# Optimization experiments

Measured on AMD Instinct MI355X. Metric: run time of the kernel, lower is better.

The kernel has to match this reference:

```python
import jax, jax.numpy as jnp
import numpy as np

N_NODES = 100000
N_EDGES = 3200000
D_IN = 128
D_HID = 128
N_CLASSES = 40


def setup_inputs() -> dict:
    key = jax.random.key(0)
    ks = jax.random.split(key, 8)
    x = jax.random.normal(ks[0], (N_NODES, D_IN), dtype=jnp.float32)
    edge_index = jax.random.randint(ks[1], (2, N_EDGES), 0, N_NODES, dtype=jnp.int64)
    s1 = 1.0 / np.sqrt(D_IN)
    s2 = 1.0 / np.sqrt(D_HID)
    W1 = jax.random.normal(ks[2], (D_IN, D_HID), dtype=jnp.float32) * s1
    b1 = jnp.zeros((D_HID,), dtype=jnp.float32)
    W2 = jax.random.normal(ks[3], (D_HID, D_HID), dtype=jnp.float32) * s2
    b2 = jnp.zeros((D_HID,), dtype=jnp.float32)
    Wl = jax.random.normal(ks[4], (D_HID, N_CLASSES), dtype=jnp.float32) * s2
    bl = jnp.zeros((N_CLASSES,), dtype=jnp.float32)
    return {"x": x, "edge_index": edge_index, "W1": W1, "b1": b1,
            "W2": W2, "b2": b2, "Wl": Wl, "bl": bl}


def _gcn_conv(x, W, b, src, dst, inv_sqrt_deg, n_nodes):
    # h = X @ W  (linear transform first: cheaper when out_dim <= in_dim)
    h = x @ W  # [N, d_out]
    # symmetric normalization: norm_e = deg(src)^-1/2 * deg(dst)^-1/2
    norm = inv_sqrt_deg[src] * inv_sqrt_deg[dst]  # [E]
    msg = h[src] * norm[:, None]                  # gather + scale  [E, d_out]
    out = jax.ops.segment_sum(msg, dst, num_segments=n_nodes)  # scatter-add
    return out + b


def reference(x, edge_index, W1, b1, W2, b2, Wl, bl):
    n = x.shape[0]
    # GCNConv adds self-loops before normalization (PyG default)
    loops = jnp.arange(n, dtype=edge_index.dtype)
    src = jnp.concatenate([edge_index[0], loops])
    dst = jnp.concatenate([edge_index[1], loops])
    deg = jax.ops.segment_sum(jnp.ones_like(dst, dtype=x.dtype), dst, num_segments=n)
    inv_sqrt_deg = jnp.where(deg > 0, jax.lax.rsqrt(deg), 0.0)

    h = _gcn_conv(x, W1, b1, src, dst, inv_sqrt_deg, n)
    h = jax.nn.relu(h)
    h = _gcn_conv(h, W2, b2, src, dst, inv_sqrt_deg, n)
    h = jax.nn.relu(h)
    return h @ Wl + bl
```

## Files before the change

### kernel.cpp

```cpp
#include <hip/hip_runtime.h>
#include <hip/hip_bf16.h>

typedef _Float16 f16;
typedef _Float16 f16x8 __attribute__((ext_vector_type(8)));

#define D 128
#define N_CLS 40
#define BN 128
#define NBMAX 1024

__global__ __launch_bounds__(256) void k_hist(const int* __restrict__ dst,
                                              int* __restrict__ bcnt, int e) {
  __shared__ int lh[NBMAX];
  for (int j = threadIdx.x; j < NBMAX; j += 256) lh[j] = 0;
  __syncthreads();
  int stride = gridDim.x * blockDim.x;
  for (int q = blockIdx.x * blockDim.x + threadIdx.x; q < e; q += stride)
    atomicAdd(&lh[dst[q] >> 7], 1);
  __syncthreads();
  for (int j = threadIdx.x; j < NBMAX; j += 256)
    if (lh[j]) atomicAdd(&bcnt[j], lh[j]);
}

__global__ __launch_bounds__(1024) void k_bscan(const int* __restrict__ bcnt,
                                                int* __restrict__ bbase,
                                                int* __restrict__ bcur) {
  __shared__ int sums[NBMAX];
  int t = threadIdx.x;
  int c = bcnt[t];
  sums[t] = c;
  __syncthreads();
  for (int off = 1; off < NBMAX; off <<= 1) {
    int a = (t >= off) ? sums[t - off] : 0;
    __syncthreads();
    sums[t] += a;
    __syncthreads();
  }
  bbase[t] = sums[t] - c;
  bcur[t] = sums[t] - c;
}

__global__ __launch_bounds__(256) void k_place(const int* __restrict__ src,
                                               const int* __restrict__ dst,
                                               int* __restrict__ bcur,
                                               unsigned int* __restrict__ binned,
                                               int e, int nwg) {
  __shared__ int lh[NBMAX];
  __shared__ int lofs[NBMAX];
  __shared__ int lcur[NBMAX];
  int chunk = (e + nwg - 1) / nwg;
  int lo = blockIdx.x * chunk;
  int hi = min(e, lo + chunk);
  int t = threadIdx.x;
  for (int j = t; j < NBMAX; j += 256) { lh[j] = 0; lcur[j] = 0; }
  __syncthreads();
  for (int q = lo + t; q < hi; q += 256) atomicAdd(&lh[dst[q] >> 7], 1);
  __syncthreads();
  for (int j = t; j < NBMAX; j += 256) {
    int c = lh[j];
    lofs[j] = c ? atomicAdd(&bcur[j], c) : 0;
  }
  __syncthreads();
  for (int q = lo + t; q < hi; q += 256) {
    int d = dst[q];
    int b = d >> 7;
    int r = atomicAdd(&lcur[b], 1);
    binned[lofs[b] + r] = ((unsigned int)(d & 127) << 17) | (unsigned int)src[q];
  }
}

__global__ __launch_bounds__(256) void k_csr(const unsigned int* __restrict__ binned,
                                             const int* __restrict__ bbase,
                                             int* __restrict__ csr,
                                             int* __restrict__ deg,
                                             float* __restrict__ isd,
                                             int* __restrict__ row_start, int n) {
  int b = blockIdx.x;
  int lo = bbase[b], hi = bbase[b + 1];
  __shared__ int h[BN];
  __shared__ int sc[BN];
  __shared__ int cur[BN];
  int t = threadIdx.x;
  if (t < BN) h[t] = 0;
  __syncthreads();
  for (int q = lo + t; q < hi; q += 256) atomicAdd(&h[binned[q] >> 17], 1);
  __syncthreads();
  if (t < BN) sc[t] = h[t];
  __syncthreads();
  for (int off = 1; off < BN; off <<= 1) {
    int a = 0;
    if (t < BN && t >= off) a = sc[t - off];
    __syncthreads();
    if (t < BN) sc[t] += a;
    __syncthreads();
  }
  if (t < BN) {
    int excl = sc[t] - h[t];
    cur[t] = lo + excl;
    int i = b * BN + t;
    if (i < n) {
      deg[i] = h[t];
      isd[i] = rsqrtf((float)(h[t] + 1));
      row_start[i] = lo + excl;
    }
  }
  __syncthreads();
  for (int q = lo + t; q < hi; q += 256) {
    unsigned int u = binned[q];
    int p = atomicAdd(&cur[u >> 17], 1);
    csr[p] = (int)(u & 0x1FFFF);
  }
}

template <bool HALF_IN>
__global__ __launch_bounds__(256) void k_gemm_t(const void* __restrict__ Xv,
                                                const float* __restrict__ W,
                                                const float* __restrict__ isd,
                                                f16* __restrict__ HS, int n) {
  __shared__ float Xt[64][D + 4];
  __shared__ float Wb[32][D + 4];
  int t = threadIdx.x;
  int r0 = blockIdx.x * 64;
  if (!HALF_IN) {
    const float* X = (const float*)Xv;
    for (int q = t; q < 64 * 32; q += 256) {
      int row = q >> 5, cb = (q & 31) << 2;
      float4 v = {0.f, 0.f, 0.f, 0.f};
      if (r0 + row < n) v = *(const float4*)(X + (size_t)(r0 + row) * D + cb);
      *(float4*)&Xt[row][cb] = v;
    }
  } else {
    const f16* X = (const f16*)Xv;
    for (int q = t; q < 64 * 16; q += 256) {
      int row = q >> 4, cb = (q & 15) << 3;
      f16x8 v = 0;
      if (r0 + row < n) v = *(const f16x8*)(X + (size_t)(r0 + row) * D + cb);
      float* xp = &Xt[row][cb];
#pragma unroll
      for (int j = 0; j < 8; ++j) xp[j] = (float)v[j];
    }
  }
  int tr = ((t >> 4) & 15) << 2;
  int tc = (t & 15) << 3;
  float acc[4][8];
#pragma unroll
  for (int i = 0; i < 4; ++i)
#pragma unroll
    for (int j = 0; j < 8; ++j) acc[i][j] = 0.f;

  for (int hh = 0; hh < 4; ++hh) {
    __syncthreads();
    for (int q = t; q < 32 * 32; q += 256) {
      int row = q >> 5, cb = (q & 31) << 2;
      *(float4*)&Wb[row][cb] = *(const float4*)(W + (size_t)(hh * 32 + row) * D + cb);
    }
    __syncthreads();
#pragma unroll 4
    for (int k = 0; k < 32; ++k) {
      float4 u0 = *(const float4*)&Wb[k][tc];
      float4 u1 = *(const float4*)&Wb[k][tc + 4];
      float bv[8] = {u0.x, u0.y, u0.z, u0.w, u1.x, u1.y, u1.z, u1.w};
      int kk = hh * 32 + k;
#pragma unroll
      for (int i = 0; i < 4; ++i) {
        float a = Xt[tr + i][kk];
#pragma unroll
        for (int j = 0; j < 8; ++j) acc[i][j] += a * bv[j];
      }
    }
  }
#pragma unroll
  for (int i = 0; i < 4; ++i) {
    int row = r0 + tr + i;
    if (row < n) {
      float s = isd[row];
      f16x8 ov;
#pragma unroll
      for (int j = 0; j < 8; ++j) ov[j] = (f16)(s * acc[i][j]);
      *(f16x8*)(HS + (size_t)row * D + tc) = ov;
    }
  }
}

__device__ inline void gather8(const f16* __restrict__ HS,
                               const int* __restrict__ csr,
                               int start, int c, int lane, float acc[8]) {
  int g = lane >> 4;
  int l = lane & 15;
  const char* base = (const char*)HS;
  size_t lofs = (size_t)(l << 4);
#pragma unroll
  for (int j = 0; j < 8; ++j) acc[j] = 0.f;

  for (int e0 = 0; e0 < c; e0 += 64) {
    int nb = min(64, c - e0);
    int idx = (lane < nb) ? csr[start + e0 + lane] : 0;
    int kb = 0;
    for (; kb + 16 <= nb; kb += 16) {
      f16x8 a16 = 0;
#pragma unroll
      for (int k = 0; k < 16; k += 4) {
        int s = __shfl(idx, kb + k + g);
        a16 += *(const f16x8*)(base + (((size_t)s) << 8) + lofs);
      }
#pragma unroll
      for (int j = 0; j < 8; ++j) acc[j] += (float)a16[j];
    }
    if (kb < nb) {
      f16x8 a16 = 0;
      for (int k = kb; k < nb; k += 4) {
        int kk = k + g;
        int s = __shfl(idx, kk);
        f16x8 u = *(const f16x8*)(base + (((size_t)s) << 8) + lofs);
        if (kk < nb) a16 += u;
      }
#pragma unroll
      for (int j = 0; j < 8; ++j) acc[j] += (float)a16[j];
    }
  }
#pragma unroll
  for (int j = 0; j < 8; ++j) {
    float v = acc[j];
    v += __shfl_xor(v, 16);
    v += __shfl_xor(v, 32);
    acc[j] = v;
  }
}

__global__ __launch_bounds__(64) void k_agg1(const f16* __restrict__ HS,
                                             const int* __restrict__ csr,
                                             const int* __restrict__ row_start,
                                             const int* __restrict__ deg,
                                             const float* __restrict__ isd,
                                             const float* __restrict__ bias,
                                             f16* __restrict__ G) {
  int i = blockIdx.x;
  int lane = threadIdx.x;
  int l = lane & 15;
  float acc[8];
  gather8(HS, csr, row_start[i], deg[i], lane, acc);
  f16x8 sv = *(const f16x8*)(HS + (size_t)i * D + l * 8);
  float di = isd[i];
  float4 bb0 = *(const float4*)(bias + l * 8);
  float4 bb1 = *(const float4*)(bias + l * 8 + 4);
  float bv[8] = {bb0.x, bb0.y, bb0.z, bb0.w, bb1.x, bb1.y, bb1.z, bb1.w};
  f16x8 ov;
#pragma unroll
  for (int j = 0; j < 8; ++j) {
    float v = di * (acc[j] + (float)sv[j]) + bv[j];
    v = v > 0.f ? v : 0.f;
    ov[j] = (f16)v;
  }
  if ((lane >> 4) == 0) *(f16x8*)(G + (size_t)i * D + l * 8) = ov;
}

__global__ __launch_bounds__(64) void k_agg_cls(const f16* __restrict__ HS,
                                                const int* __restrict__ csr,
                                                const int* __restrict__ row_start,
                                                const int* __restrict__ deg,
                                                const float* __restrict__ isd,
                                                const float* __restrict__ b2,
                                                const float* __restrict__ Wl,
                                                const float* __restrict__ bl,
                                                float* __restrict__ out) {
  int i = blockIdx.x;
  int lane = threadIdx.x;
  int l = lane & 15;
  float acc[8];
  gather8(HS, csr, row_start[i], deg[i], lane, acc);
  f16x8 sv = *(const f16x8*)(HS + (size_t)i * D + l * 8);
  float di = isd[i];
  float4 bb0 = *(const float4*)(b2 + l * 8);
  float4 bb1 = *(const float4*)(b2 + l * 8 + 4);
  float bv[8] = {bb0.x, bb0.y, bb0.z, bb0.w, bb1.x, bb1.y, bb1.z, bb1.w};
  __shared__ float tt[D];
#pragma unroll
  for (int j = 0; j < 8; ++j) {
    float v = di * (acc[j] + (float)sv[j]) + bv[j];
    bv[j] = v > 0.f ? v : 0.f;
  }
  if ((lane >> 4) == 0) {
    *(float4*)&tt[l * 8] = make_float4(bv[0], bv[1], bv[2], bv[3]);
    *(float4*)&tt[l * 8 + 4] = make_float4(bv[4], bv[5], bv[6], bv[7]);
  }
  __syncthreads();
  if (lane < N_CLS) {
    float o = bl[lane];
#pragma unroll 8
    for (int k = 0; k < D; ++k) o += tt[k] * Wl[k * N_CLS + lane];
    out[(size_t)i * N_CLS + lane] = o;
  }
}

extern "C" void kernel_launch(void* const* d_in, const int* in_sizes, int n_in,
                              void* d_out, int out_size, void* d_ws, size_t ws_size,
                              hipStream_t stream) {
  const float* x  = (const float*)d_in[0];
  const int*   ei = (const int*)d_in[1];
  const float* W1 = (const float*)d_in[2];
  const float* b1 = (const float*)d_in[3];
  const float* W2 = (const float*)d_in[4];
  const float* b2 = (const float*)d_in[5];
  const float* Wl = (const float*)d_in[6];
  const float* bl = (const float*)d_in[7];
  float* out = (float*)d_out;

  const int n = in_sizes[0] / D;
  const int e = in_sizes[1] / 2;
  const int* src = ei;
  const int* dst = ei + e;
  const int nb = (n + BN - 1) / BN;

  char* ws = (char*)d_ws;
  size_t off = 0;
  auto alloc = [&](size_t bytes) -> void* {
    void* p = ws + off;
    off += (bytes + 255) & ~(size_t)255;
    return p;
  };
  int*   bcnt      = (int*)alloc(NBMAX * 4);
  int*   bbase     = (int*)alloc(NBMAX * 4);
  int*   bcur      = (int*)alloc(NBMAX * 4);
  int*   deg       = (int*)alloc((size_t)n * 4);
  int*   row_start = (int*)alloc((size_t)n * 4);
  float* isd       = (float*)alloc((size_t)n * 4);
  int*   csr       = (int*)alloc((size_t)e * 4);
  f16*   hA        = (f16*)alloc((size_t)n * D * 2);
  f16*   hB        = (f16*)alloc((size_t)n * D * 2);
  unsigned int* binned = (unsigned int*)hA;

  hipMemsetAsync(bcnt, 0, NBMAX * 4, stream);

  const int nwg_place = 512;
  k_hist<<<1024, 256, 0, stream>>>(dst, bcnt, e);
  k_bscan<<<1, 1024, 0, stream>>>(bcnt, bbase, bcur);
  k_place<<<nwg_place, 256, 0, stream>>>(src, dst, bcur, binned, e, nwg_place);
  k_csr<<<nb, 256, 0, stream>>>(binned, bbase, csr, deg, isd, row_start, n);

  int gblocks = (n + 63) / 64;
  k_gemm_t<false><<<gblocks, 256, 0, stream>>>(x, W1, isd, hA, n);
  k_agg1<<<n, 64, 0, stream>>>(hA, csr, row_start, deg, isd, b1, hB);
  k_gemm_t<true><<<gblocks, 256, 0, stream>>>(hB, W2, isd, hA, n);
  k_agg_cls<<<n, 64, 0, stream>>>(hA, csr, row_start, deg, isd, b2, Wl, bl, out);
}
```

Measured before the change: 570.3 us.

## Rework gather to issue 8 independent row loads per lane, pack 4 nodes per block

The neighbor gather no longer loads 64 indices cooperatively and broadcasts them by shuffle. Each lane now reads its own 8 CSR indices directly, using clamped addresses, then issues 8 independent 16-byte row loads before summing in fp16 pairs. This raises memory-level parallelism per wave for average degree about 33. Both aggregation kernels now pack 4 nodes (one per wave) into 256-thread blocks, and the classifier loop reads the shared hidden vector as float4. The trade-offs are more redundant index loads, loads wasted on partial tails, and fp16 partial sums of 4 values before conversion to fp32.

```diff
diff --git a/kernel.cpp b/kernel.cpp
--- a/kernel.cpp
+++ b/kernel.cpp
@@ -185,64 +185,59 @@
 __device__ inline void gather8(const f16* __restrict__ HS,
                                const int* __restrict__ csr,
                                int start, int c, int lane, float acc[8]) {
-  int g = lane >> 4;
+  const int g = lane >> 4;
+  const char* base = (const char*)HS + ((lane & 15) << 4);
+  const int* __restrict__ cp = csr + start;
+#pragma unroll
+  for (int j = 0; j < 8; ++j) acc[j] = 0.f;
+
+  for (int u = 0; u < c; u += 32) {
+    int eg = u + g;
+    int ec = c - 1;
+    int sA[8];
+#pragma unroll
+    for (int k = 0; k < 8; ++k) {
+      int ee = eg + (k << 2);
+      sA[k] = cp[ee < ec ? ee : ec];
+    }
+    f16x8 v[8];
+#pragma unroll
+    for (int k = 0; k < 8; ++k) {
+      v[k] = (f16x8)0;
+      if (eg + (k << 2) < c)
+        v[k] = *(const f16x8*)(base + ((size_t)(unsigned)sA[k] << 8));
+    }
+    f16x8 A = (v[0] + v[1]) + (v[2] + v[3]);
+    f16x8 B = (v[4] + v[5]) + (v[6] + v[7]);
+#pragma unroll
+    for (int j = 0; j < 8; ++j) acc[j] += (float)A[j] + (float)B[j];
+  }
+#pragma unroll
+  for (int j = 0; j < 8; ++j) {
+    float t = acc[j];
+    t += __shfl_xor(t, 16);
+    t += __shfl_xor(t, 32);
+    acc[j] = t;
+  }
+}
+
+__global__ __launch_bounds__(256) void k_agg1(const f16* __restrict__ HS,
+                                              const int* __restrict__ csr,
+                                              const int* __restrict__ row_start,
+                                              const int* __restrict__ deg,
+                                              const float* __restrict__ isd,
+                                              const float* __restrict__ bias,
+                                              f16* __restrict__ G, int n) {
+  int i = (blockIdx.x << 2) + (threadIdx.x >> 6);
+  if (i >= n) return;
+  int lane = threadIdx.x & 63;
   int l = lane & 15;
-  const char* base = (const char*)HS;
-  size_t lofs = (size_t)(l << 4);
-#pragma unroll
-  for (int j = 0; j < 8; ++j) acc[j] = 0.f;
-
-  for (int e0 = 0; e0 < c; e0 += 64) {
-    int nb = min(64, c - e0);
-    int idx = (lane < nb) ? csr[start + e0 + lane] : 0;
-    int kb = 0;
-    for (; kb + 16 <= nb; kb += 16) {
-      f16x8 a16 = 0;
-#pragma unroll
-      for (int k = 0; k < 16; k += 4) {
-        int s = __shfl(idx, kb + k + g);
-        a16 += *(const f16x8*)(base + (((size_t)s) << 8) + lofs);
-      }
-#pragma unroll
-      for (int j = 0; j < 8; ++j) acc[j] += (float)a16[j];
-    }
-    if (kb < nb) {
-      f16x8 a16 = 0;
-      for (int k = kb; k < nb; k += 4) {
-        int kk = k + g;
-        int s = __shfl(idx, kk);
-        f16x8 u = *(const f16x8*)(base + (((size_t)s) << 8) + lofs);
-        if (kk < nb) a16 += u;
-      }
-#pragma unroll
-      for (int j = 0; j < 8; ++j) acc[j] += (float)a16[j];
-    }
-  }
-#pragma unroll
-  for (int j = 0; j < 8; ++j) {
-    float v = acc[j];
-    v += __shfl_xor(v, 16);
-    v += __shfl_xor(v, 32);
-    acc[j] = v;
-  }
-}
-
-__global__ __launch_bounds__(64) void k_agg1(const f16* __restrict__ HS,
-                                             const int* __restrict__ csr,
-                                             const int* __restrict__ row_start,
-                                             const int* __restrict__ deg,
-                                             const float* __restrict__ isd,
-                                             const float* __restrict__ bias,
-                                             f16* __restrict__ G) {
-  int i = blockIdx.x;
-  int lane = threadIdx.x;
-  int l = lane & 15;
-  float acc[8];
-  gather8(HS, csr, row_start[i], deg[i], lane, acc);
   f16x8 sv = *(const f16x8*)(HS + (size_t)i * D + l * 8);
   float di = isd[i];
   float4 bb0 = *(const float4*)(bias + l * 8);
   float4 bb1 = *(const float4*)(bias + l * 8 + 4);
+  float acc[8];
+  gather8(HS, csr, row_start[i], deg[i], lane, acc);
   float bv[8] = {bb0.x, bb0.y, bb0.z, bb0.w, bb1.x, bb1.y, bb1.z, bb1.w};
   f16x8 ov;
 #pragma unroll
@@ -254,41 +249,49 @@
   if ((lane >> 4) == 0) *(f16x8*)(G + (size_t)i * D + l * 8) = ov;
 }
 
-__global__ __launch_bounds__(64) void k_agg_cls(const f16* __restrict__ HS,
-                                                const int* __restrict__ csr,
-                                                const int* __restrict__ row_start,
-                                                const int* __restrict__ deg,
-                                                const float* __restrict__ isd,
-                                                const float* __restrict__ b2,
-                                                const float* __restrict__ Wl,
-                                                const float* __restrict__ bl,
-                                                float* __restrict__ out) {
-  int i = blockIdx.x;
-  int lane = threadIdx.x;
+__global__ __launch_bounds__(256) void k_agg_cls(const f16* __restrict__ HS,
+                                                 const int* __restrict__ csr,
+                                                 const int* __restrict__ row_start,
+                                                 const int* __restrict__ deg,
+                                                 const float* __restrict__ isd,
+                                                 const float* __restrict__ b2,
+                                                 const float* __restrict__ Wl,
+                                                 const float* __restrict__ bl,
+                                                 float* __restrict__ out, int n) {
+  int wv = threadIdx.x >> 6;
+  int ir = (blockIdx.x << 2) + wv;
+  int i = ir < n ? ir : n - 1;
+  int lane = threadIdx.x & 63;
   int l = lane & 15;
-  float acc[8];
-  gather8(HS, csr, row_start[i], deg[i], lane, acc);
   f16x8 sv = *(const f16x8*)(HS + (size_t)i * D + l * 8);
   float di = isd[i];
   float4 bb0 = *(const float4*)(b2 + l * 8);
   float4 bb1 = *(const float4*)(b2 + l * 8 + 4);
+  float acc[8];
+  gather8(HS, csr, row_start[i], deg[i], lane, acc);
   float bv[8] = {bb0.x, bb0.y, bb0.z, bb0.w, bb1.x, bb1.y, bb1.z, bb1.w};
-  __shared__ float tt[D];
+  __shared__ float tt[4][D];
 #pragma unroll
   for (int j = 0; j < 8; ++j) {
     float v = di * (acc[j] + (float)sv[j]) + bv[j];
     bv[j] = v > 0.f ? v : 0.f;
   }
   if ((lane >> 4) == 0) {
-    *(float4*)&tt[l * 8] = make_float4(bv[0], bv[1], bv[2], bv[3]);
-    *(float4*)&tt[l * 8 + 4] = make_float4(bv[4], bv[5], bv[6], bv[7]);
-  }
-  __syncthreads();
-  if (lane < N_CLS) {
+    *(float4*)&tt[wv][l * 8] = make_float4(bv[0], bv[1], bv[2], bv[3]);
+    *(float4*)&tt[wv][l * 8 + 4] = make_float4(bv[4], bv[5], bv[6], bv[7]);
+  }
+  __syncthreads();
+  if (ir < n && lane < N_CLS) {
     float o = bl[lane];
-#pragma unroll 8
-    for (int k = 0; k < D; ++k) o += tt[k] * Wl[k * N_CLS + lane];
-    out[(size_t)i * N_CLS + lane] = o;
+#pragma unroll 4
+    for (int k = 0; k < D; k += 4) {
+      float4 t4 = *(const float4*)&tt[wv][k];
+      o += t4.x * Wl[(size_t)(k + 0) * N_CLS + lane];
+      o += t4.y * Wl[(size_t)(k + 1) * N_CLS + lane];
+      o += t4.z * Wl[(size_t)(k + 2) * N_CLS + lane];
+      o += t4.w * Wl[(size_t)(k + 3) * N_CLS + lane];
+    }
+    out[(size_t)ir * N_CLS + lane] = o;
   }
 }
 
@@ -338,8 +341,9 @@
   k_csr<<<nb, 256, 0, stream>>>(binned, bbase, csr, deg, isd, row_start, n);
 
   int gblocks = (n + 63) / 64;
+  int ablocks = (n + 3) / 4;
   k_gemm_t<false><<<gblocks, 256, 0, stream>>>(x, W1, isd, hA, n);
-  k_agg1<<<n, 64, 0, stream>>>(hA, csr, row_start, deg, isd, b1, hB);
+  k_agg1<<<ablocks, 256, 0, stream>>>(hA, csr, row_start, deg, isd, b1, hB, n);
   k_gemm_t<true><<<gblocks, 256, 0, stream>>>(hB, W2, isd, hA, n);
-  k_agg_cls<<<n, 64, 0, stream>>>(hA, csr, row_start, deg, isd, b2, Wl, bl, out);
-}
+  k_agg_cls<<<ablocks, 256, 0, stream>>>(hA, csr, row_start, deg, isd, b2, Wl, bl, out, n);
+}
```

Measured after the change: 569.2 us. About the same (-0.2%).
